# Kernel optimization log

Measured on AMD Instinct MI355X. Metric: run time of the kernel, lower is better.

The kernel has to match this reference:

```python
import jax, jax.numpy as jnp
import numpy as np

B, T, C = 2, 2048, 1024
H = 16
D = C // H
SCALE = 0.1 / (D ** 0.5)  # nonstandard 0.1/sqrt(head_dim) scale from source


def setup_inputs() -> dict:
    key = jax.random.key(0)
    ks = jax.random.split(key, 5)
    s = 0.02
    return {
        "x": jax.random.normal(ks[0], (B, T, C), jnp.float32),
        "w_attn": jax.random.normal(ks[1], (C, 3 * C), jnp.float32) * s,
        "b_attn": jax.random.normal(ks[2], (3 * C,), jnp.float32) * s,
        "w_proj": jax.random.normal(ks[3], (C, C), jnp.float32) * s,
        "b_proj": jax.random.normal(ks[4], (C,), jnp.float32) * s,
    }


def reference(x, w_attn, b_attn, w_proj, b_proj):
    Bs, Ts, Cs = x.shape
    qkv = x @ w_attn + b_attn                      # [B,T,3C]
    q, k, v = jnp.split(qkv, 3, axis=-1)
    q = q.reshape(Bs, Ts, H, D)                    # [B,T,H,D]
    k = k.reshape(Bs, Ts, H, D)
    v = v.reshape(Bs, Ts, H, D)
    attn = jnp.einsum("bthd,bshd->bhts", q, k) * SCALE  # [B,H,T,T]
    causal = jnp.tril(jnp.ones((Ts, Ts), dtype=bool))
    attn = jnp.where(causal, attn, -jnp.inf)
    attn = jax.nn.softmax(attn, axis=-1)
    y = jnp.einsum("bhts,bshd->bthd", attn, v).reshape(Bs, Ts, Cs)
    return y @ w_proj + b_proj
```

## Files before the change

### kernel.cpp

```cpp
#include <hip/hip_runtime.h>


#define Bz 2
#define Tz 2048
#define Cz 1024
#define Hz 16
#define Dz 64
#define QSCALE 0.01803368801111437f

typedef unsigned short u16;
typedef short bf16x4 __attribute__((ext_vector_type(4)));
typedef short bf16x8 __attribute__((ext_vector_type(8)));
typedef float f32x4 __attribute__((ext_vector_type(4)));

#define MFMA32(A, B, C) __builtin_amdgcn_mfma_f32_16x16x32_bf16(A, B, C, 0, 0, 0)

__device__ inline f32x4 mfma16(bf16x4 a, bf16x4 b, f32x4 c) {
#if defined(__HIP_DEVICE_COMPILE__)
  return __builtin_amdgcn_mfma_f32_16x16x16bf16_1k(a, b, c, 0, 0, 0);
#else
  return c;
#endif
}

__device__ inline u16 f2bf(float f) {
  return (u16)((__float_as_uint(f) + 0x8000u) >> 16);
}

__device__ inline float fexp2(float x) {
#if __has_builtin(__builtin_amdgcn_exp2f)
  return __builtin_amdgcn_exp2f(x);
#else
  return exp2f(x);
#endif
}

__device__ inline void gl_lds16(const u16* g, u16* l) {
  __builtin_amdgcn_global_load_lds(
      (const __attribute__((address_space(1))) void*)g,
      (__attribute__((address_space(3))) void*)l, 16, 0, 0);
}

#define NCAST 4096
#define NTA   3072
__global__ __launch_bounds__(256) void prep_kernel(const float* __restrict__ x,
                                                   const float* __restrict__ wa,
                                                   const float* __restrict__ wp,
                                                   u16* __restrict__ xb,
                                                   u16* __restrict__ waT,
                                                   u16* __restrict__ wpT) {
  const int bx = blockIdx.x, t = threadIdx.x;
  if (bx < NCAST) {
    int i = bx * 256 + t;
    float4 v = ((const float4*)x)[i];
    ushort4 o = {f2bf(v.x), f2bf(v.y), f2bf(v.z), f2bf(v.w)};
    ((ushort4*)xb)[i] = o;
    return;
  }
  __shared__ float tile[32][33];
  const float* W;
  u16* WT;
  int N, idx;
  if (bx < NCAST + NTA) {
    W = wa; WT = waT; N = 3 * Cz; idx = bx - NCAST;
  } else {
    W = wp; WT = wpT; N = Cz; idx = bx - NCAST - NTA;
  }
  const int n0 = (idx % (N / 32)) * 32, k0 = (idx / (N / 32)) * 32;
  const int tx = t & 31, ty = t >> 5;
#pragma unroll
  for (int i = 0; i < 4; ++i)
    tile[ty + 8 * i][tx] = W[(size_t)(k0 + ty + 8 * i) * N + n0 + tx];
  __syncthreads();
#pragma unroll
  for (int i = 0; i < 4; ++i)
    WT[(size_t)(n0 + ty + 8 * i) * Cz + k0 + tx] = f2bf(tile[tx][ty + 8 * i]);
}

__global__ __launch_bounds__(512, 2) void gemm_qkv(const u16* __restrict__ A,
                                                   const u16* __restrict__ BT,
                                                   const float* __restrict__ bias,
                                                   u16* __restrict__ Cout,
                                                   u16* __restrict__ vTout) {
  constexpr int K = Cz;
  constexpr int N = 3 * Cz;
  constexpr int KT = K / 64;
  __shared__ __align__(16) u16 L[2][4][128 * 64];

  const int t = threadIdx.x;
  const int wave = t >> 6, lane = t & 63;
  const int lm = lane & 15, lg = lane >> 4;
  const int wm = wave >> 2, wn = wave & 3;
  const int m0 = blockIdx.y * 256, n0 = blockIdx.x * 256;

  const int srow = 8 * wave + (lane >> 3);
  const int sgl = ((lane & 7) ^ (lane >> 3)) * 8;

  auto stage_ht = [&](int kt, int ht) {
    const bool isA = (ht == 0) || (ht == 3);
    const int half = (ht >= 2) ? 1 : 0;
    const u16* src =
        (isA ? A + (size_t)(m0 + half * 128 + srow) * K
             : BT + (size_t)(n0 + half * 128 + srow) * K) +
        (size_t)kt * 64 + sgl;
    u16* dst = &L[kt & 1][ht][(8 * wave) * 64];
    gl_lds16(src, dst);
    gl_lds16(src + (size_t)64 * K, dst + 64 * 64);
  };

  f32x4 acc[2][2][4][2];
#pragma unroll
  for (int qa = 0; qa < 2; ++qa)
#pragma unroll
    for (int qb = 0; qb < 2; ++qb)
#pragma unroll
      for (int mt = 0; mt < 4; ++mt)
#pragma unroll
        for (int nt = 0; nt < 2; ++nt)
#pragma unroll
          for (int i = 0; i < 4; ++i) acc[qa][qb][mt][nt][i] = 0.f;

#pragma unroll
  for (int i = 0; i < 4; ++i) stage_ht(0, i);
  asm volatile("s_waitcnt vmcnt(4)" ::: "memory");
  __builtin_amdgcn_s_barrier();

  for (int kt = 0; kt < KT; ++kt) {
    const int cb = kt & 1;
#pragma unroll
    for (int ph = 0; ph < 4; ++ph) {
      const int qa = ph >> 1, qb = ph & 1;
      bf16x8 af[4][2], bfr[2][2];
#pragma unroll
      for (int mt = 0; mt < 4; ++mt)
#pragma unroll
        for (int h = 0; h < 2; ++h)
          af[mt][h] = *(const bf16x8*)&L[cb][qa ? 3 : 0]
              [(64 * wm + 16 * mt + lm) * 64 + (((lg + 4 * h) ^ (lm & 7)) << 3)];
#pragma unroll
      for (int nt = 0; nt < 2; ++nt)
#pragma unroll
        for (int h = 0; h < 2; ++h)
          bfr[nt][h] = *(const bf16x8*)&L[cb][qb ? 2 : 1]
              [(32 * wn + 16 * nt + lm) * 64 + (((lg + 4 * h) ^ (lm & 7)) << 3)];
      if (kt + 1 < KT) stage_ht(kt + 1, ph);
      __builtin_amdgcn_s_barrier();
      asm volatile("s_waitcnt lgkmcnt(0)" ::: "memory");
      __builtin_amdgcn_s_setprio(1);
#pragma unroll
      for (int mt = 0; mt < 4; ++mt)
#pragma unroll
        for (int nt = 0; nt < 2; ++nt) {
          acc[qa][qb][mt][nt] = MFMA32(af[mt][0], bfr[nt][0], acc[qa][qb][mt][nt]);
          acc[qa][qb][mt][nt] = MFMA32(af[mt][1], bfr[nt][1], acc[qa][qb][mt][nt]);
        }
      __builtin_amdgcn_s_setprio(0);
      if (kt < KT - 1)
        asm volatile("s_waitcnt vmcnt(4)" ::: "memory");
      else if (ph == 0)
        asm volatile("s_waitcnt vmcnt(2)" ::: "memory");
      else
        asm volatile("s_waitcnt vmcnt(0)" ::: "memory");
      __builtin_amdgcn_s_barrier();
    }
  }

#pragma unroll
  for (int qa = 0; qa < 2; ++qa)
#pragma unroll
    for (int qb = 0; qb < 2; ++qb)
#pragma unroll
      for (int nt = 0; nt < 2; ++nt) {
        const int gc = n0 + 128 * qb + 32 * wn + 16 * nt + lm;
        const float bv = bias[gc];
        if (gc >= 2 * Cz) {
          const int dg = gc - 2 * Cz;
#pragma unroll
          for (int mt = 0; mt < 4; ++mt) {
            const int gr0 = m0 + 128 * qa + 64 * wm + 16 * mt + 4 * lg;
            const int bb = gr0 >> 11, s0 = gr0 & 2047;
            const f32x4 av = acc[qa][qb][mt][nt];
            ushort4 o = {f2bf(av[0] + bv), f2bf(av[1] + bv),
                         f2bf(av[2] + bv), f2bf(av[3] + bv)};
            *(ushort4*)(vTout + (((size_t)(bb * 1024 + dg)) << 11) + s0) = o;
          }
        } else {
          const float sc = (gc < Cz) ? QSCALE : 1.f;
#pragma unroll
          for (int mt = 0; mt < 4; ++mt)
#pragma unroll
            for (int i = 0; i < 4; ++i) {
              const int gr = m0 + 128 * qa + 64 * wm + 16 * mt + 4 * lg + i;
              Cout[(size_t)gr * N + gc] = f2bf((acc[qa][qb][mt][nt][i] + bv) * sc);
            }
        }
      }
}

template <bool OUT_BF16, int TN, bool VSPLIT>
__global__ __launch_bounds__(256) void gemm_bt(const u16* __restrict__ A,
                                               const u16* __restrict__ BT,
                                               const float* __restrict__ bias,
                                               void* __restrict__ Cout,
                                               u16* __restrict__ vTout,
                                               int M, int N, int K,
                                               int qcols, float qscale) {
  __shared__ __align__(16) u16 As[128 * 64];
  __shared__ __align__(16) u16 Bs[TN * 64];
  constexpr int NT = TN / 32;
  const int t = threadIdx.x;
  const int wave = t >> 6, lane = t & 63;
  const int lm = lane & 15, lg = lane >> 4;
  const int wm = wave >> 1, wn = wave & 1;
  const int m0 = blockIdx.y * 128, n0 = blockIdx.x * TN;

  const int lrow = lane >> 3;
  const int gseg = (lane & 7) ^ lrow;
  const size_t a_base = (size_t)(m0 + 32 * wave + lrow) * K + gseg * 8;
  u16* const a_lds = &As[(32 * wave) * 64];
  const size_t b_base = (size_t)(n0 + (TN / 4) * wave + lrow) * K + gseg * 8;
  u16* const b_lds = &Bs[((TN / 4) * wave) * 64];

  f32x4 acc[4][NT];
#pragma unroll
  for (int mt = 0; mt < 4; ++mt)
#pragma unroll
    for (int nt = 0; nt < NT; ++nt)
#pragma unroll
      for (int i = 0; i < 4; ++i) acc[mt][nt][i] = 0.f;

  for (int k0 = 0; k0 < K; k0 += 64) {
    __syncthreads();
#pragma unroll
    for (int i = 0; i < 4; ++i)
      gl_lds16(A + a_base + (size_t)(8 * i) * K + k0, a_lds + i * 8 * 64);
#pragma unroll
    for (int i = 0; i < NT; ++i)
      gl_lds16(BT + b_base + (size_t)(8 * i) * K + k0, b_lds + i * 8 * 64);
    __syncthreads();

#pragma unroll
    for (int h = 0; h < 2; ++h) {
      const int rs = ((lg + 4 * h) ^ (lm & 7)) * 8;
      bf16x8 af[4], bfr[NT];
#pragma unroll
      for (int mt = 0; mt < 4; ++mt)
        af[mt] = *(const bf16x8*)&As[(64 * wm + 16 * mt + lm) * 64 + rs];
#pragma unroll
      for (int nt = 0; nt < NT; ++nt)
        bfr[nt] = *(const bf16x8*)&Bs[((TN / 2) * wn + 16 * nt + lm) * 64 + rs];
#pragma unroll
      for (int mt = 0; mt < 4; ++mt)
#pragma unroll
        for (int nt = 0; nt < NT; ++nt)
          acc[mt][nt] = MFMA32(af[mt], bfr[nt], acc[mt][nt]);
    }
  }

#pragma unroll
  for (int nt = 0; nt < NT; ++nt) {
    int gc = n0 + (TN / 2) * wn + 16 * nt + lm;
    float bv = bias[gc];
    if (VSPLIT && gc >= 2 * Cz) {
      const int dg = gc - 2 * Cz;
#pragma unroll
      for (int mt = 0; mt < 4; ++mt) {
        const int gr0 = m0 + 64 * wm + 16 * mt + 4 * lg;
        const int bb = gr0 >> 11, s0 = gr0 & 2047;
        ushort4 o = {f2bf(acc[mt][nt][0] + bv), f2bf(acc[mt][nt][1] + bv),
                     f2bf(acc[mt][nt][2] + bv), f2bf(acc[mt][nt][3] + bv)};
        *(ushort4*)(vTout + (((size_t)(bb * 1024 + dg)) << 11) + s0) = o;
      }
      continue;
    }
    float sc = (gc < qcols) ? qscale : 1.f;
#pragma unroll
    for (int mt = 0; mt < 4; ++mt) {
#pragma unroll
      for (int i = 0; i < 4; ++i) {
        int gr = m0 + 64 * wm + 16 * mt + 4 * lg + i;
        float v = (acc[mt][nt][i] + bv) * sc;
        if (OUT_BF16)
          ((u16*)Cout)[(size_t)gr * N + gc] = f2bf(v);
        else
          ((float*)Cout)[(size_t)gr * N + gc] = v;
      }
    }
  }
}

__global__ __launch_bounds__(256) void attn_kernel(const u16* __restrict__ qkv,
                                                   const u16* __restrict__ vT,
                                                   u16* __restrict__ yb) {
  __shared__ __align__(16) u16 KsL[2][64 * 64];
  __shared__ __align__(16) u16 VtL[2][64 * 64];

  const int t = threadIdx.x;
  const int wave = t >> 6, lane = t & 63;
  const int lm = lane & 15, lg = lane >> 4;
  const int x = blockIdx.x;
  const int bh = x & 31, qtp = x >> 5;
  const int qt = (qtp < 16) ? qtp : 47 - qtp;
  const int b = bh >> 4, h = bh & 15;
  const int q0 = qt * 64;
  const size_t rowstride = 3 * Cz;
  const u16* qbase = qkv + (size_t)b * Tz * rowstride + h * Dz;
  const u16* vTbh = vT + ((size_t)(b * Hz + h) * Dz) * Tz;

  bf16x8 qf[2];
  {
    const u16* qrow = qbase + (size_t)(q0 + wave * 16 + lm) * rowstride + (lg << 3);
    qf[0] = *(const bf16x8*)qrow;
    qf[1] = *(const bf16x8*)(qrow + 32);
  }

  float psum = 0.f;
  f32x4 Oa[4];
#pragma unroll
  for (int i = 0; i < 4; ++i)
#pragma unroll
    for (int j = 0; j < 4; ++j) Oa[i][j] = 0.f;

  const int srow = lane >> 3;
  const int sgl = ((lane & 7) ^ srow) * 8;
  const u16* kstg = qbase + Cz + (size_t)(16 * wave + srow) * rowstride + sgl;
  const u16* vstg = vTbh + (size_t)(16 * wave + srow) * Tz + sgl;

  auto stage_issue = [&](int kt, int buf) {
#pragma unroll
    for (int c2 = 0; c2 < 2; ++c2) {
      gl_lds16(kstg + (size_t)(8 * c2) * rowstride + (size_t)(64 * kt) * rowstride,
               &KsL[buf][(16 * wave + 8 * c2) * 64]);
      gl_lds16(vstg + (size_t)(8 * c2) * Tz + 64 * kt,
               &VtL[buf][(16 * wave + 8 * c2) * 64]);
    }
  };

  stage_issue(0, 0);

  for (int kt = 0; kt <= qt; ++kt) {
    __syncthreads();
    const int cb = kt & 1;
    if (kt + 1 <= qt) stage_issue(kt + 1, 1 - cb);

    f32x4 S[4];
#pragma unroll
    for (int c = 0; c < 4; ++c) {
      const int rb = (16 * c + lm) * 64;
      bf16x8 k0 = *(const bf16x8*)&KsL[cb][rb + ((lg ^ (lm & 7)) << 3)];
      bf16x8 k1 = *(const bf16x8*)&KsL[cb][rb + (((lg + 4) ^ (lm & 7)) << 3)];
      f32x4 s;
#pragma unroll
      for (int i = 0; i < 4; ++i) s[i] = 0.f;
      s = MFMA32(k0, qf[0], s);
      s = MFMA32(k1, qf[1], s);
      S[c] = s;
    }

    const bool diag = (kt == qt);
    const int qloc = 16 * wave + lm;
    bf16x4 pf[4];
#pragma unroll
    for (int c = 0; c < 4; ++c) {
#pragma unroll
      for (int r = 0; r < 4; ++r) {
        float p = fexp2(S[c][r]);
        if (diag && (c * 16 + 4 * lg + r) > qloc) p = 0.f;
        psum += p;
        pf[c][r] = (short)f2bf(p);
      }
    }

#pragma unroll
    for (int dt = 0; dt < 4; ++dt) {
      const int rb = (16 * dt + lm) * 64;
#pragma unroll
      for (int c = 0; c < 4; ++c) {
        const int off = (((2 * c + (lg >> 1)) ^ (lm & 7)) << 3) + 4 * (lg & 1);
        bf16x4 vfr = *(const bf16x4*)&VtL[cb][rb + off];
        Oa[dt] = mfma16(pf[c], vfr, Oa[dt]);
      }
    }
  }

  float s = psum;
  s += __shfl_xor(s, 16);
  s += __shfl_xor(s, 32);
  const float linv = 1.f / s;
  float invq[4];
#pragma unroll
  for (int r = 0; r < 4; ++r)
    invq[r] = __shfl(linv, 20 * lg + r);
  __syncthreads();
#pragma unroll
  for (int dt = 0; dt < 4; ++dt)
#pragma unroll
    for (int r = 0; r < 4; ++r)
      KsL[0][(16 * wave + 4 * lg + r) * 64 + 16 * dt + lm] =
          f2bf(Oa[dt][r] * invq[r]);
  __syncthreads();
  {
    const int row = lane >> 2, seg = lane & 3;
    const uint4* src = (const uint4*)&KsL[0][(16 * wave + row) * 64 + seg * 16];
    uint4 v0 = src[0];
    uint4 v1 = src[1];
    u16* dst = yb + (size_t)(b * Tz + q0 + 16 * wave + row) * Cz + h * Dz + seg * 16;
    *(uint4*)dst = v0;
    *(uint4*)(dst + 8) = v1;
  }
}

extern "C" void kernel_launch(void* const* d_in, const int* in_sizes, int n_in,
                              void* d_out, int out_size, void* d_ws, size_t ws_size,
                              hipStream_t stream) {
  const float* x      = (const float*)d_in[0];
  const float* w_attn = (const float*)d_in[1];
  const float* b_attn = (const float*)d_in[2];
  const float* w_proj = (const float*)d_in[3];
  const float* b_proj = (const float*)d_in[4];

  char* ws = (char*)d_ws;
  u16* xb   = (u16*)(ws);
  u16* waT  = (u16*)(ws + (8ull << 20));
  u16* wpT  = (u16*)(ws + (14ull << 20));
  u16* qkvb = (u16*)(ws + (16ull << 20));
  u16* yb   = (u16*)(ws + (40ull << 20));
  u16* vTt  = (u16*)(ws + (48ull << 20));

  const int M = Bz * Tz;

  prep_kernel<<<NCAST + NTA + 1024, 256, 0, stream>>>(x, w_attn, w_proj, xb, waT, wpT);
  gemm_qkv<<<dim3(3 * Cz / 256, M / 256), 512, 0, stream>>>(xb, waT, b_attn, qkvb, vTt);
  attn_kernel<<<1024, 256, 0, stream>>>(qkvb, vTt, yb);
  gemm_bt<false, 64, false><<<dim3(Cz / 64, M / 128), 256, 0, stream>>>(
      yb, wpT, b_proj, d_out, nullptr, M, Cz, Cz, 0, 1.f);
}
```

Baseline: 177.6 us.

## Restructure QKV GEMM pipeline with fragment reuse, bulk staging, and block swizzle

The QKV GEMM main loop now issues all global-to-LDS loads for the next k-tile at once. It reuses the A and B fragments across the four quadrant MFMA phases instead of reloading both operands every phase, and peels the final iteration. Block indices are remapped with an XCD-aware swizzle (8 groups of 24) to improve L2 locality across chiplets. This reduces LDS reads and makes the barriers and waitcnt schedule less uniform, at the cost of more registers live at once and hand-tuned vmcnt values that must match the load order.

```diff
diff --git a/kernel.cpp b/kernel.cpp
--- a/kernel.cpp
+++ b/kernel.cpp
@@ -91,21 +91,31 @@
   const int wave = t >> 6, lane = t & 63;
   const int lm = lane & 15, lg = lane >> 4;
   const int wm = wave >> 2, wn = wave & 3;
-  const int m0 = blockIdx.y * 256, n0 = blockIdx.x * 256;
+
+  const int bid = blockIdx.y * 12 + blockIdx.x;
+  const int swz = (bid & 7) * 24 + (bid >> 3);
+  const int m0 = (swz / 12) * 256, n0 = (swz % 12) * 256;
 
   const int srow = 8 * wave + (lane >> 3);
   const int sgl = ((lane & 7) ^ (lane >> 3)) * 8;
-
-  auto stage_ht = [&](int kt, int ht) {
-    const bool isA = (ht == 0) || (ht == 3);
-    const int half = (ht >= 2) ? 1 : 0;
-    const u16* src =
-        (isA ? A + (size_t)(m0 + half * 128 + srow) * K
-             : BT + (size_t)(n0 + half * 128 + srow) * K) +
-        (size_t)kt * 64 + sgl;
-    u16* dst = &L[kt & 1][ht][(8 * wave) * 64];
-    gl_lds16(src, dst);
-    gl_lds16(src + (size_t)64 * K, dst + 64 * 64);
+  const u16* aS = A + (size_t)(m0 + srow) * K + sgl;
+  const u16* bS = BT + (size_t)(n0 + srow) * K + sgl;
+
+  auto stage_all = [&](int kt) {
+    const int b = kt & 1;
+    const size_t ko = (size_t)kt * 64;
+    u16* d0 = &L[b][0][(8 * wave) * 64];
+    gl_lds16(aS + ko, d0);
+    gl_lds16(aS + ko + (size_t)64 * K, d0 + 64 * 64);
+    u16* d1 = &L[b][1][(8 * wave) * 64];
+    gl_lds16(bS + ko, d1);
+    gl_lds16(bS + ko + (size_t)64 * K, d1 + 64 * 64);
+    u16* d2 = &L[b][2][(8 * wave) * 64];
+    gl_lds16(bS + ko + (size_t)128 * K, d2);
+    gl_lds16(bS + ko + (size_t)192 * K, d2 + 64 * 64);
+    u16* d3 = &L[b][3][(8 * wave) * 64];
+    gl_lds16(aS + ko + (size_t)128 * K, d3);
+    gl_lds16(aS + ko + (size_t)192 * K, d3 + 64 * 64);
   };
 
   f32x4 acc[2][2][4][2];
@@ -120,49 +130,147 @@
 #pragma unroll
           for (int i = 0; i < 4; ++i) acc[qa][qb][mt][nt][i] = 0.f;
 
-#pragma unroll
-  for (int i = 0; i < 4; ++i) stage_ht(0, i);
+  const int roff0 = (lg ^ (lm & 7)) << 3;
+  const int roff1 = ((lg + 4) ^ (lm & 7)) << 3;
+  const int arow = (64 * wm + lm) * 64;
+  const int brow = (32 * wn + lm) * 64;
+
+  stage_all(0);
   asm volatile("s_waitcnt vmcnt(4)" ::: "memory");
   __builtin_amdgcn_s_barrier();
 
-  for (int kt = 0; kt < KT; ++kt) {
+  for (int kt = 0; kt < KT - 1; ++kt) {
     const int cb = kt & 1;
-#pragma unroll
-    for (int ph = 0; ph < 4; ++ph) {
-      const int qa = ph >> 1, qb = ph & 1;
-      bf16x8 af[4][2], bfr[2][2];
-#pragma unroll
-      for (int mt = 0; mt < 4; ++mt)
-#pragma unroll
-        for (int h = 0; h < 2; ++h)
-          af[mt][h] = *(const bf16x8*)&L[cb][qa ? 3 : 0]
-              [(64 * wm + 16 * mt + lm) * 64 + (((lg + 4 * h) ^ (lm & 7)) << 3)];
-#pragma unroll
-      for (int nt = 0; nt < 2; ++nt)
-#pragma unroll
-        for (int h = 0; h < 2; ++h)
-          bfr[nt][h] = *(const bf16x8*)&L[cb][qb ? 2 : 1]
-              [(32 * wn + 16 * nt + lm) * 64 + (((lg + 4 * h) ^ (lm & 7)) << 3)];
-      if (kt + 1 < KT) stage_ht(kt + 1, ph);
-      __builtin_amdgcn_s_barrier();
-      asm volatile("s_waitcnt lgkmcnt(0)" ::: "memory");
-      __builtin_amdgcn_s_setprio(1);
-#pragma unroll
-      for (int mt = 0; mt < 4; ++mt)
-#pragma unroll
-        for (int nt = 0; nt < 2; ++nt) {
-          acc[qa][qb][mt][nt] = MFMA32(af[mt][0], bfr[nt][0], acc[qa][qb][mt][nt]);
-          acc[qa][qb][mt][nt] = MFMA32(af[mt][1], bfr[nt][1], acc[qa][qb][mt][nt]);
-        }
-      __builtin_amdgcn_s_setprio(0);
-      if (kt < KT - 1)
-        asm volatile("s_waitcnt vmcnt(4)" ::: "memory");
-      else if (ph == 0)
-        asm volatile("s_waitcnt vmcnt(2)" ::: "memory");
-      else
-        asm volatile("s_waitcnt vmcnt(0)" ::: "memory");
-      __builtin_amdgcn_s_barrier();
-    }
+    const u16* Lc = &L[cb][0][0];
+    bf16x8 af[4][2], bfr[2][2][2];
+#pragma unroll
+    for (int mt = 0; mt < 4; ++mt) {
+      af[mt][0] = *(const bf16x8*)&Lc[0 * 8192 + arow + 16 * mt * 64 + roff0];
+      af[mt][1] = *(const bf16x8*)&Lc[0 * 8192 + arow + 16 * mt * 64 + roff1];
+    }
+#pragma unroll
+    for (int nt = 0; nt < 2; ++nt) {
+      bfr[0][nt][0] = *(const bf16x8*)&Lc[1 * 8192 + brow + 16 * nt * 64 + roff0];
+      bfr[0][nt][1] = *(const bf16x8*)&Lc[1 * 8192 + brow + 16 * nt * 64 + roff1];
+    }
+    stage_all(kt + 1);
+    __builtin_amdgcn_s_barrier();
+    asm volatile("s_waitcnt lgkmcnt(0)" ::: "memory");
+    __builtin_amdgcn_s_setprio(1);
+#pragma unroll
+    for (int mt = 0; mt < 4; ++mt)
+#pragma unroll
+      for (int nt = 0; nt < 2; ++nt) {
+        acc[0][0][mt][nt] = MFMA32(af[mt][0], bfr[0][nt][0], acc[0][0][mt][nt]);
+        acc[0][0][mt][nt] = MFMA32(af[mt][1], bfr[0][nt][1], acc[0][0][mt][nt]);
+      }
+    __builtin_amdgcn_s_setprio(0);
+    asm volatile("s_waitcnt vmcnt(10)" ::: "memory");
+    __builtin_amdgcn_s_barrier();
+#pragma unroll
+    for (int nt = 0; nt < 2; ++nt) {
+      bfr[1][nt][0] = *(const bf16x8*)&Lc[2 * 8192 + brow + 16 * nt * 64 + roff0];
+      bfr[1][nt][1] = *(const bf16x8*)&Lc[2 * 8192 + brow + 16 * nt * 64 + roff1];
+    }
+    __builtin_amdgcn_s_barrier();
+    asm volatile("s_waitcnt lgkmcnt(0)" ::: "memory");
+    __builtin_amdgcn_s_setprio(1);
+#pragma unroll
+    for (int mt = 0; mt < 4; ++mt)
+#pragma unroll
+      for (int nt = 0; nt < 2; ++nt) {
+        acc[0][1][mt][nt] = MFMA32(af[mt][0], bfr[1][nt][0], acc[0][1][mt][nt]);
+        acc[0][1][mt][nt] = MFMA32(af[mt][1], bfr[1][nt][1], acc[0][1][mt][nt]);
+      }
+    __builtin_amdgcn_s_setprio(0);
+    asm volatile("s_waitcnt vmcnt(8)" ::: "memory");
+    __builtin_amdgcn_s_barrier();
+#pragma unroll
+    for (int mt = 0; mt < 4; ++mt) {
+      af[mt][0] = *(const bf16x8*)&Lc[3 * 8192 + arow + 16 * mt * 64 + roff0];
+      af[mt][1] = *(const bf16x8*)&Lc[3 * 8192 + arow + 16 * mt * 64 + roff1];
+    }
+    __builtin_amdgcn_s_barrier();
+    asm volatile("s_waitcnt lgkmcnt(0)" ::: "memory");
+    __builtin_amdgcn_s_setprio(1);
+#pragma unroll
+    for (int mt = 0; mt < 4; ++mt)
+#pragma unroll
+      for (int nt = 0; nt < 2; ++nt) {
+        acc[1][0][mt][nt] = MFMA32(af[mt][0], bfr[0][nt][0], acc[1][0][mt][nt]);
+        acc[1][0][mt][nt] = MFMA32(af[mt][1], bfr[0][nt][1], acc[1][0][mt][nt]);
+      }
+    __builtin_amdgcn_s_setprio(0);
+    __builtin_amdgcn_s_barrier();
+    __builtin_amdgcn_s_setprio(1);
+#pragma unroll
+    for (int mt = 0; mt < 4; ++mt)
+#pragma unroll
+      for (int nt = 0; nt < 2; ++nt) {
+        acc[1][1][mt][nt] = MFMA32(af[mt][0], bfr[1][nt][0], acc[1][1][mt][nt]);
+        acc[1][1][mt][nt] = MFMA32(af[mt][1], bfr[1][nt][1], acc[1][1][mt][nt]);
+      }
+    __builtin_amdgcn_s_setprio(0);
+    asm volatile("s_waitcnt vmcnt(4)" ::: "memory");
+    __builtin_amdgcn_s_barrier();
+  }
+
+  {
+    const int cb = (KT - 1) & 1;
+    const u16* Lc = &L[cb][0][0];
+    bf16x8 af[4][2], bfr[2][2][2];
+#pragma unroll
+    for (int mt = 0; mt < 4; ++mt) {
+      af[mt][0] = *(const bf16x8*)&Lc[0 * 8192 + arow + 16 * mt * 64 + roff0];
+      af[mt][1] = *(const bf16x8*)&Lc[0 * 8192 + arow + 16 * mt * 64 + roff1];
+    }
+#pragma unroll
+    for (int nt = 0; nt < 2; ++nt) {
+      bfr[0][nt][0] = *(const bf16x8*)&Lc[1 * 8192 + brow + 16 * nt * 64 + roff0];
+      bfr[0][nt][1] = *(const bf16x8*)&Lc[1 * 8192 + brow + 16 * nt * 64 + roff1];
+    }
+    __builtin_amdgcn_s_barrier();
+    asm volatile("s_waitcnt lgkmcnt(0)" ::: "memory");
+#pragma unroll
+    for (int mt = 0; mt < 4; ++mt)
+#pragma unroll
+      for (int nt = 0; nt < 2; ++nt) {
+        acc[0][0][mt][nt] = MFMA32(af[mt][0], bfr[0][nt][0], acc[0][0][mt][nt]);
+        acc[0][0][mt][nt] = MFMA32(af[mt][1], bfr[0][nt][1], acc[0][0][mt][nt]);
+      }
+    asm volatile("s_waitcnt vmcnt(2)" ::: "memory");
+    __builtin_amdgcn_s_barrier();
+#pragma unroll
+    for (int nt = 0; nt < 2; ++nt) {
+      bfr[1][nt][0] = *(const bf16x8*)&Lc[2 * 8192 + brow + 16 * nt * 64 + roff0];
+      bfr[1][nt][1] = *(const bf16x8*)&Lc[2 * 8192 + brow + 16 * nt * 64 + roff1];
+    }
+    __builtin_amdgcn_s_barrier();
+    asm volatile("s_waitcnt lgkmcnt(0)" ::: "memory");
+#pragma unroll
+    for (int mt = 0; mt < 4; ++mt)
+#pragma unroll
+      for (int nt = 0; nt < 2; ++nt) {
+        acc[0][1][mt][nt] = MFMA32(af[mt][0], bfr[1][nt][0], acc[0][1][mt][nt]);
+        acc[0][1][mt][nt] = MFMA32(af[mt][1], bfr[1][nt][1], acc[0][1][mt][nt]);
+      }
+    asm volatile("s_waitcnt vmcnt(0)" ::: "memory");
+    __builtin_amdgcn_s_barrier();
+#pragma unroll
+    for (int mt = 0; mt < 4; ++mt) {
+      af[mt][0] = *(const bf16x8*)&Lc[3 * 8192 + arow + 16 * mt * 64 + roff0];
+      af[mt][1] = *(const bf16x8*)&Lc[3 * 8192 + arow + 16 * mt * 64 + roff1];
+    }
+    asm volatile("s_waitcnt lgkmcnt(0)" ::: "memory");
+#pragma unroll
+    for (int mt = 0; mt < 4; ++mt)
+#pragma unroll
+      for (int nt = 0; nt < 2; ++nt) {
+        acc[1][0][mt][nt] = MFMA32(af[mt][0], bfr[0][nt][0], acc[1][0][mt][nt]);
+        acc[1][0][mt][nt] = MFMA32(af[mt][1], bfr[0][nt][1], acc[1][0][mt][nt]);
+        acc[1][1][mt][nt] = MFMA32(af[mt][0], bfr[1][nt][0], acc[1][1][mt][nt]);
+        acc[1][1][mt][nt] = MFMA32(af[mt][1], bfr[1][nt][1], acc[1][1][mt][nt]);
+      }
   }
 
 #pragma unroll
@@ -430,7 +538,7 @@
   const int M = Bz * Tz;
 
   prep_kernel<<<NCAST + NTA + 1024, 256, 0, stream>>>(x, w_attn, w_proj, xb, waT, wpT);
-  gemm_qkv<<<dim3(3 * Cz / 256, M / 256), 512, 0, stream>>>(xb, waT, b_attn, qkvb, vTt);
+  gemm_qkv<<<dim3(12, 16), 512, 0, stream>>>(xb, waT, b_attn, qkvb, vTt);
   attn_kernel<<<1024, 256, 0, stream>>>(qkvb, vTt, yb);
   gemm_bt<false, 64, false><<<dim3(Cz / 64, M / 128), 256, 0, stream>>>(
       yb, wpT, b_proj, d_out, nullptr, M, Cz, Cz, 0, 1.f);
```

After: 176.4 us. No clear change (-0.7%).

## Reschedule QKV GEMM main loop with deeper prefetch, fragment reuse, and block swizzle

Applied to the files above, without the earlier changes.

Rewrites the QKV GEMM inner loop as a hand-scheduled two-k-tile unrolled pipeline. Loads for the next tile are issued further ahead (seven stages in flight), and A/B fragments are reused across quadrants in a snake order (00,01,11,10) to cut LDS reads. It also remaps block IDs so that consecutive blocks, which are dispatched across the 8 XCDs, cover neighbouring tiles and share L2 data. The aim is to hide global-load latency and lower LDS traffic. The cost is a complex waitcnt/barrier schedule that is easy to get wrong.

```diff
diff --git a/kernel.cpp b/kernel.cpp
--- a/kernel.cpp
+++ b/kernel.cpp
@@ -91,19 +91,20 @@
   const int wave = t >> 6, lane = t & 63;
   const int lm = lane & 15, lg = lane >> 4;
   const int wm = wave >> 2, wn = wave & 3;
-  const int m0 = blockIdx.y * 256, n0 = blockIdx.x * 256;
+
+  const int bid = blockIdx.y * 12 + blockIdx.x;
+  const int swz = (bid & 7) * 24 + (bid >> 3);
+  const int m0 = (swz / 12) * 256, n0 = (swz % 12) * 256;
 
   const int srow = 8 * wave + (lane >> 3);
   const int sgl = ((lane & 7) ^ (lane >> 3)) * 8;
 
-  auto stage_ht = [&](int kt, int ht) {
-    const bool isA = (ht == 0) || (ht == 3);
-    const int half = (ht >= 2) ? 1 : 0;
-    const u16* src =
-        (isA ? A + (size_t)(m0 + half * 128 + srow) * K
-             : BT + (size_t)(n0 + half * 128 + srow) * K) +
-        (size_t)kt * 64 + sgl;
-    u16* dst = &L[kt & 1][ht][(8 * wave) * 64];
+  auto stage = [&](int kt, int rg) {
+    const u16* src = (rg == 0 || rg == 3)
+        ? A + (size_t)(m0 + ((rg == 3) ? 128 : 0) + srow) * K
+        : BT + (size_t)(n0 + ((rg == 2) ? 128 : 0) + srow) * K;
+    src += (size_t)kt * 64 + sgl;
+    u16* dst = &L[kt & 1][rg][(8 * wave) * 64];
     gl_lds16(src, dst);
     gl_lds16(src + (size_t)64 * K, dst + 64 * 64);
   };
@@ -120,50 +121,87 @@
 #pragma unroll
           for (int i = 0; i < 4; ++i) acc[qa][qb][mt][nt][i] = 0.f;
 
-#pragma unroll
-  for (int i = 0; i < 4; ++i) stage_ht(0, i);
-  asm volatile("s_waitcnt vmcnt(4)" ::: "memory");
-  __builtin_amdgcn_s_barrier();
-
-  for (int kt = 0; kt < KT; ++kt) {
-    const int cb = kt & 1;
-#pragma unroll
-    for (int ph = 0; ph < 4; ++ph) {
-      const int qa = ph >> 1, qb = ph & 1;
-      bf16x8 af[4][2], bfr[2][2];
-#pragma unroll
-      for (int mt = 0; mt < 4; ++mt)
-#pragma unroll
-        for (int h = 0; h < 2; ++h)
-          af[mt][h] = *(const bf16x8*)&L[cb][qa ? 3 : 0]
-              [(64 * wm + 16 * mt + lm) * 64 + (((lg + 4 * h) ^ (lm & 7)) << 3)];
-#pragma unroll
-      for (int nt = 0; nt < 2; ++nt)
-#pragma unroll
-        for (int h = 0; h < 2; ++h)
-          bfr[nt][h] = *(const bf16x8*)&L[cb][qb ? 2 : 1]
-              [(32 * wn + 16 * nt + lm) * 64 + (((lg + 4 * h) ^ (lm & 7)) << 3)];
-      if (kt + 1 < KT) stage_ht(kt + 1, ph);
-      __builtin_amdgcn_s_barrier();
-      asm volatile("s_waitcnt lgkmcnt(0)" ::: "memory");
-      __builtin_amdgcn_s_setprio(1);
-#pragma unroll
-      for (int mt = 0; mt < 4; ++mt)
-#pragma unroll
-        for (int nt = 0; nt < 2; ++nt) {
-          acc[qa][qb][mt][nt] = MFMA32(af[mt][0], bfr[nt][0], acc[qa][qb][mt][nt]);
-          acc[qa][qb][mt][nt] = MFMA32(af[mt][1], bfr[nt][1], acc[qa][qb][mt][nt]);
-        }
-      __builtin_amdgcn_s_setprio(0);
-      if (kt < KT - 1)
-        asm volatile("s_waitcnt vmcnt(4)" ::: "memory");
-      else if (ph == 0)
-        asm volatile("s_waitcnt vmcnt(2)" ::: "memory");
-      else
-        asm volatile("s_waitcnt vmcnt(0)" ::: "memory");
-      __builtin_amdgcn_s_barrier();
-    }
-  }
+  const int roff0 = (lg ^ (lm & 7)) << 3;
+  const int roff1 = ((lg + 4) ^ (lm & 7)) << 3;
+  const int arow = (64 * wm + lm) * 64;
+  const int brow = (32 * wn + lm) * 64;
+
+  bf16x8 af[4][2], bfr[2][2][2];
+
+#define RD_A(BUF, RG)                                                         \
+  _Pragma("unroll") for (int mt = 0; mt < 4; ++mt) {                          \
+    af[mt][0] = *(const bf16x8*)&L[BUF][RG][arow + 1024 * mt + roff0];        \
+    af[mt][1] = *(const bf16x8*)&L[BUF][RG][arow + 1024 * mt + roff1];        \
+  }
+#define RD_B(BUF, RG, QB)                                                     \
+  _Pragma("unroll") for (int nt = 0; nt < 2; ++nt) {                          \
+    bfr[QB][nt][0] = *(const bf16x8*)&L[BUF][RG][brow + 1024 * nt + roff0];   \
+    bfr[QB][nt][1] = *(const bf16x8*)&L[BUF][RG][brow + 1024 * nt + roff1];   \
+  }
+#define DO_MFMA(QA, QB)                                                       \
+  __builtin_amdgcn_s_setprio(1);                                             \
+  _Pragma("unroll") for (int mt = 0; mt < 4; ++mt)                            \
+      _Pragma("unroll") for (int nt = 0; nt < 2; ++nt) {                      \
+    acc[QA][QB][mt][nt] =                                                     \
+        MFMA32(af[mt][0], bfr[QB][nt][0], acc[QA][QB][mt][nt]);               \
+    acc[QA][QB][mt][nt] =                                                     \
+        MFMA32(af[mt][1], bfr[QB][nt][1], acc[QA][QB][mt][nt]);               \
+  }                                                                           \
+  __builtin_amdgcn_s_setprio(0);
+#define BAR __builtin_amdgcn_s_barrier()
+#define WVM(NN) asm volatile("s_waitcnt vmcnt(" #NN ")" ::: "memory")
+#define WLG(NN) asm volatile("s_waitcnt lgkmcnt(" #NN ")" ::: "memory")
+
+  stage(0, 0); stage(0, 1); stage(0, 2); stage(0, 3);
+  stage(1, 0); stage(1, 1); stage(1, 2);
+  WVM(10);
+  BAR;
+
+  for (int i = 0; i < KT / 2 - 1; ++i) {
+    const int t1 = 2 * i + 1, t2 = 2 * i + 2, t3 = 2 * i + 3;
+    RD_A(0, 0) RD_B(0, 1, 0) stage(t1, 3);
+    WLG(8);
+    BAR; WLG(0); DO_MFMA(0, 0) WVM(10); BAR;
+    RD_B(0, 2, 1) stage(t2, 0);
+    BAR; WLG(0); DO_MFMA(0, 1) WVM(10); BAR;
+    RD_A(0, 3) stage(t2, 1);
+    BAR; WLG(0); DO_MFMA(1, 1) WVM(10); BAR;
+    stage(t2, 2);
+    BAR; DO_MFMA(1, 0) WVM(10); BAR;
+    RD_A(1, 0) RD_B(1, 1, 0) stage(t2, 3);
+    WLG(8);
+    BAR; WLG(0); DO_MFMA(0, 0) WVM(10); BAR;
+    RD_B(1, 2, 1) stage(t3, 0);
+    BAR; WLG(0); DO_MFMA(0, 1) WVM(10); BAR;
+    RD_A(1, 3) stage(t3, 1);
+    BAR; WLG(0); DO_MFMA(1, 1) WVM(10); BAR;
+    stage(t3, 2);
+    BAR; DO_MFMA(1, 0) WVM(10); BAR;
+  }
+
+  {
+    RD_A(0, 0) RD_B(0, 1, 0) stage(KT - 1, 3);
+    WLG(8);
+    BAR; WLG(0); DO_MFMA(0, 0) WVM(8); BAR;
+    RD_B(0, 2, 1)
+    BAR; WLG(0); DO_MFMA(0, 1) WVM(8); BAR;
+    RD_A(0, 3)
+    BAR; WLG(0); DO_MFMA(1, 1) BAR;
+    BAR; DO_MFMA(1, 0) WVM(4); BAR;
+    RD_A(1, 0) RD_B(1, 1, 0)
+    BAR; WLG(0); DO_MFMA(0, 0) WVM(2); BAR;
+    RD_B(1, 2, 1)
+    BAR; WLG(0); DO_MFMA(0, 1) WVM(0); BAR;
+    RD_A(1, 3)
+    BAR; WLG(0); DO_MFMA(1, 1)
+    DO_MFMA(1, 0)
+  }
+#undef RD_A
+#undef RD_B
+#undef DO_MFMA
+#undef BAR
+#undef WVM
+#undef WLG
 
 #pragma unroll
   for (int qa = 0; qa < 2; ++qa)
@@ -430,7 +468,7 @@
   const int M = Bz * Tz;
 
   prep_kernel<<<NCAST + NTA + 1024, 256, 0, stream>>>(x, w_attn, w_proj, xb, waT, wpT);
-  gemm_qkv<<<dim3(3 * Cz / 256, M / 256), 512, 0, stream>>>(xb, waT, b_attn, qkvb, vTt);
+  gemm_qkv<<<dim3(12, 16), 512, 0, stream>>>(xb, waT, b_attn, qkvb, vTt);
   attn_kernel<<<1024, 256, 0, stream>>>(qkvb, vTt, yb);
   gemm_bt<false, 64, false><<<dim3(Cz / 64, M / 128), 256, 0, stream>>>(
       yb, wpT, b_proj, d_out, nullptr, M, Cz, Cz, 0, 1.f);
```

Result: faster. 171.9 us (-3.2%).
